# Kernel tuning notes

Hardware: AMD Instinct MI355X
Metric: run time of the kernel (lower is better)

## Reference

```python
import jax, jax.numpy as jnp
import numpy as np

H = 56; W = 56; WS = 7; SHIFT = 3; C = 256; NH = 8
HD = C // NH; N = WS * WS; NW = (H // WS) * (W // WS)
SCALE = HD ** -0.5
LN_EPS = 1e-5


def _rel_pos_index():
    coords = np.stack(np.meshgrid(np.arange(WS), np.arange(WS), indexing='ij'))  # (2, ws, ws)
    cf = coords.reshape(2, -1)
    rel = (cf[:, :, None] - cf[:, None, :]).transpose(1, 2, 0)  # (N, N, 2)
    rel[..., 0] += WS - 1
    rel[..., 1] += WS - 1
    rel[..., 0] *= 2 * WS - 1
    return rel.sum(-1)  # (N, N) indices into (2*ws-1)^2 table

RPI = jnp.asarray(_rel_pos_index())


def _attn_mask():
    img = np.zeros((H, W))
    slices = (slice(0, -WS), slice(-WS, -SHIFT), slice(-SHIFT, None))
    cnt = 0
    for hs in slices:
        for ws_ in slices:
            img[hs, ws_] = cnt
            cnt += 1
    mw = img.reshape(H // WS, WS, W // WS, WS).transpose(0, 2, 1, 3).reshape(-1, N)
    diff = mw[:, None, :] - mw[:, :, None]  # (nW, N, N), [w,i,j] = mw[w,j]-mw[w,i]
    return jnp.asarray(np.where(diff != 0, -100.0, 0.0).astype(np.float32))

AMASK = _attn_mask()  # (nW, N, N)


def ln(x, g, b):
    m = x.mean(-1, keepdims=True)
    v = x.var(-1, keepdims=True)
    return (x - m) / jnp.sqrt(v + LN_EPS) * g + b


def win_part(x):  # (B, H, W, C) -> (B*nW, N, C)
    B = x.shape[0]
    return x.reshape(B, H // WS, WS, W // WS, WS, C).transpose(0, 1, 3, 2, 4, 5).reshape(-1, N, C)


def win_rev(xw, B):  # (B*nW, N, C) -> (B, H, W, C)
    return xw.reshape(B, H // WS, W // WS, WS, WS, C).transpose(0, 1, 3, 2, 4, 5).reshape(B, H, W, C)


def setup_inputs() -> dict:
    key = jax.random.key(0)
    ks = iter(jax.random.split(key, 40))
    B, L = 16, H * W
    Ch = int(C * 4.0)
    p = {}
    p['x'] = jax.random.normal(next(ks), (B, L, C), jnp.float32)
    p['x_SAR'] = jax.random.normal(next(ks), (B, L, C), jnp.float32)
    p['ln1_g'] = jnp.ones((C,)); p['ln1_b'] = jnp.zeros((C,))
    p['ln1s_g'] = jnp.ones((C,)); p['ln1s_b'] = jnp.zeros((C,))
    p['qkv_w'] = jax.random.normal(next(ks), (3 * C, C)) * 0.02
    p['qkv_b'] = jnp.zeros((3 * C,))
    p['qkvs_w'] = jax.random.normal(next(ks), (3 * C, C)) * 0.02
    p['qkvs_b'] = jnp.zeros((3 * C,))
    p['rpb_table'] = jax.random.normal(next(ks), ((2 * WS - 1) ** 2, NH)) * 0.02
    p['fuse_w'] = jax.random.normal(next(ks), (NH, NH)) * 0.1  # Conv2d(8,8,1) weight squeezed
    p['fuse_b'] = jnp.zeros((NH,))
    p['proj_w'] = jax.random.normal(next(ks), (C, C)) * 0.02
    p['proj_b'] = jnp.zeros((C,))
    p['projs_w'] = jax.random.normal(next(ks), (C, C)) * 0.02
    p['projs_b'] = jnp.zeros((C,))
    p['ln2_g'] = jnp.ones((C,)); p['ln2_b'] = jnp.zeros((C,))
    p['ln2s_g'] = jnp.ones((C,)); p['ln2s_b'] = jnp.zeros((C,))
    p['fc1_w'] = jax.random.normal(next(ks), (Ch, C)) * 0.02
    p['fc1_b'] = jnp.zeros((Ch,))
    p['fc2_w'] = jax.random.normal(next(ks), (C, Ch)) * 0.02
    p['fc2_b'] = jnp.zeros((C,))
    p['fc1s_w'] = jax.random.normal(next(ks), (Ch, C)) * 0.02
    p['fc1s_b'] = jnp.zeros((Ch,))
    p['fc2s_w'] = jax.random.normal(next(ks), (C, Ch)) * 0.02
    p['fc2s_b'] = jnp.zeros((C,))
    return p


def reference(x, x_SAR, ln1_g, ln1_b, ln1s_g, ln1s_b, qkv_w, qkv_b, qkvs_w, qkvs_b,
              rpb_table, fuse_w, fuse_b, proj_w, proj_b, projs_w, projs_b,
              ln2_g, ln2_b, ln2s_g, ln2s_b, fc1_w, fc1_b, fc2_w, fc2_b,
              fc1s_w, fc1s_b, fc2s_w, fc2s_b):
    B = x.shape[0]
    sc, sc_s = x, x_SAR

    def pre(xx, g, b):  # norm -> spatial -> cyclic shift -> windows
        xs = ln(xx, g, b).reshape(B, H, W, C)
        xs = jnp.roll(xs, (-SHIFT, -SHIFT), axis=(1, 2))
        return win_part(xs)

    xw = pre(x, ln1_g, ln1_b)
    xws = pre(x_SAR, ln1s_g, ln1s_b)

    def qkv_f(xin, Wt, bt):
        qkv = (xin @ Wt.T + bt).reshape(-1, N, 3, NH, HD).transpose(2, 0, 3, 1, 4)
        return qkv[0], qkv[1], qkv[2]  # each (B*nW, nH, N, HD)

    q, k, v = qkv_f(xw, qkv_w, qkv_b)
    qs, ks_, vs = qkv_f(xws, qkvs_w, qkvs_b)

    attn = jnp.einsum('bhnd,bhmd->bhnm', q * SCALE, k)
    attn_s = jnp.einsum('bhnd,bhmd->bhnm', qs * SCALE, ks_)

    rpb = rpb_table[RPI.reshape(-1)].reshape(N, N, NH).transpose(2, 0, 1)  # (nH, N, N)
    attn = attn + rpb[None]
    attn_s = attn_s + rpb[None]

    # shift-window mask add
    attn = (attn.reshape(B, NW, NH, N, N) + AMASK[None, :, None]).reshape(-1, NH, N, N)
    attn_s = (attn_s.reshape(B, NW, NH, N, N) + AMASK[None, :, None]).reshape(-1, NH, N, N)

    # dual-branch fusion: 1x1 conv over head dim + sigmoid gate
    diff = attn_s - attn
    gate = jax.nn.sigmoid(jnp.einsum('oh,bhnm->bonm', fuse_w, diff) + fuse_b[None, :, None, None])
    attn_f = jax.nn.softmax(attn + diff * gate, axis=-1)
    attn_s = jax.nn.softmax(attn_s, axis=-1)

    def out_f(a, vv, pw, pb):
        o = jnp.einsum('bhnm,bhmd->bhnd', a, vv).transpose(0, 2, 1, 3).reshape(-1, N, C)
        return o @ pw.T + pb

    xo = out_f(attn_f, v, proj_w, proj_b)
    xos = out_f(attn_s, vs, projs_w, projs_b)

    def post(xout, scc, g2, b2, w1, b1, w2, b2m):
        xr = jnp.roll(win_rev(xout, B), (SHIFT, SHIFT), axis=(1, 2)).reshape(B, -1, C)
        xr = scc + xr
        h = jax.nn.gelu(ln(xr, g2, b2) @ w1.T + b1, approximate=False)
        return xr + (h @ w2.T + b2m)

    out = post(xo, sc, ln2_g, ln2_b, fc1_w, fc1_b, fc2_w, fc2_b)
    out_s = post(xos, sc_s, ln2s_g, ln2s_b, fc1s_w, fc1s_b, fc2s_w, fc2s_b)
    return out, out_s
```

## Files before the change

kernel.cpp:

```cpp
#include <hip/hip_runtime.h>
#include <hip/hip_bf16.h>
#include <cstdio>

typedef unsigned short ushort_t;
using bf16x8  = __attribute__((ext_vector_type(8))) __bf16;
using floatx4 = __attribute__((ext_vector_type(4))) float;

constexpr int    kTokens = 50176;
constexpr size_t TCsz    = (size_t)kTokens * 256;
constexpr float  kScale  = 0.17677669529663687f;
constexpr int    SPITCH  = 56;
constexpr size_t SPAIR   = 49 * 56;
constexpr size_t SBUFSZ  = (size_t)8192 * SPAIR;

__device__ __forceinline__ float bf2f(ushort_t u) {
  unsigned int x = (unsigned int)u << 16;
  return __uint_as_float(x);
}
__device__ __forceinline__ ushort_t f2bf(float f) {
  __hip_bfloat16 h = __float2bfloat16(f);
  return *(ushort_t*)&h;
}

__global__ __launch_bounds__(256) void f2b_k(const float* __restrict__ src,
                                             ushort_t* __restrict__ dst, int n) {
  int i = blockIdx.x * 256 + threadIdx.x;
  if (i < n) dst[i] = f2bf(src[i]);
}

__global__ __launch_bounds__(256) void bias_k(const float* __restrict__ rpb,
                                              float* __restrict__ bias,
                                              ushort_t* __restrict__ guard) {
  const int cls = blockIdx.x >> 3, head = blockIdx.x & 7;
  const int wh7 = cls >> 1, ww7 = cls & 1;
  float* bp = bias + (size_t)blockIdx.x * SPAIR;
  for (int e = threadIdx.x; e < (int)SPAIR; e += 256) {
    const int i = e / SPITCH, j = e % SPITCH;
    float val = 0.0f;
    if (j < 49) {
      const int yi = i / 7, xi = i % 7, yj = j / 7, xj = j % 7;
      val = rpb[((yi - yj + 6) * 13 + (xi - xj + 6)) * 8 + head];
      const int li = (wh7 ? (yi < 4 ? 1 : 2) : 0) * 3 + (ww7 ? (xi < 4 ? 1 : 2) : 0);
      const int lj = (wh7 ? (yj < 4 ? 1 : 2) : 0) * 3 + (ww7 ? (xj < 4 ? 1 : 2) : 0);
      if (li != lj) val -= 100.0f;
    }
    bp[e] = val;
  }
  if (blockIdx.x == 0 && threadIdx.x < 64) guard[threadIdx.x] = 0;
}

template <int SHIFTED>
__global__ __launch_bounds__(256) void ln_k(const float* __restrict__ x,
                                            const float* __restrict__ g,
                                            const float* __restrict__ b,
                                            ushort_t* __restrict__ yout) {
  const int wave = threadIdx.x >> 6, lane = threadIdx.x & 63;
  const int t = blockIdx.x * 4 + wave;
  size_t src;
  if (SHIFTED) {
    int bb = t / 3136, r = t % 3136;
    int wi = r / 49, n = r % 49;
    int hp = (wi >> 3) * 7 + n / 7;
    int wp = (wi & 7) * 7 + n % 7;
    int sh = hp + 3; if (sh >= 56) sh -= 56;
    int sw = wp + 3; if (sw >= 56) sw -= 56;
    src = ((size_t)bb * 3136 + sh * 56 + sw) * 256;
  } else {
    src = (size_t)t * 256;
  }
  const float4 v4 = *(const float4*)(x + src + lane * 4);
  float s  = v4.x + v4.y + v4.z + v4.w;
  float s2 = v4.x * v4.x + v4.y * v4.y + v4.z * v4.z + v4.w * v4.w;
#pragma unroll
  for (int off = 32; off > 0; off >>= 1) {
    s  += __shfl_xor(s,  off);
    s2 += __shfl_xor(s2, off);
  }
  const float mean = s * (1.0f / 256.0f);
  const float var  = s2 * (1.0f / 256.0f) - mean * mean;
  const float rstd = rsqrtf(var + 1e-5f);
  const float4 g4 = *(const float4*)(g + lane * 4);
  const float4 b4 = *(const float4*)(b + lane * 4);
  ushort4 o;
  o.x = f2bf((v4.x - mean) * rstd * g4.x + b4.x);
  o.y = f2bf((v4.y - mean) * rstd * g4.y + b4.y);
  o.z = f2bf((v4.z - mean) * rstd * g4.z + b4.z);
  o.w = f2bf((v4.w - mean) * rstd * g4.w + b4.w);
  *(ushort4*)(yout + (size_t)t * 256 + lane * 4) = o;
}

template <int MODE>
__global__ __launch_bounds__(256) void bgemm_k(const ushort_t* __restrict__ A,
                                               const ushort_t* __restrict__ W,
                                               const float* __restrict__ bias,
                                               float* __restrict__ outf,
                                               ushort_t* __restrict__ outb,
                                               const float* __restrict__ aux,
                                               int K, int Nc) {
  __shared__ __align__(16) ushort_t As[4][128][8];
  __shared__ __align__(16) ushort_t Bs[4][128][8];
  const int tid  = threadIdx.x;
  const int m0   = blockIdx.y * 128;
  const int n0   = blockIdx.x * 128;
  const int lane = tid & 63, wv = tid >> 6;
  const int wm   = (wv >> 1) * 64, wn = (wv & 1) * 64;
  const int l16  = lane & 15, quad = lane >> 4;
  const int srow = tid >> 2;
  const int skc  = tid & 3;

  floatx4 acc[4][4] = {};
  const ushort_t* Ap0 = A + (size_t)(m0 + srow) * K + skc * 8;
  const ushort_t* Ap1 = A + (size_t)(m0 + 64 + srow) * K + skc * 8;
  const ushort_t* Wp0 = W + (size_t)(n0 + srow) * K + skc * 8;
  const ushort_t* Wp1 = W + (size_t)(n0 + 64 + srow) * K + skc * 8;

  for (int k0 = 0; k0 < K; k0 += 32) {
    uint4 a0 = *(const uint4*)(Ap0 + k0);
    uint4 a1 = *(const uint4*)(Ap1 + k0);
    uint4 b0 = *(const uint4*)(Wp0 + k0);
    uint4 b1 = *(const uint4*)(Wp1 + k0);
    *(uint4*)&As[skc][srow][0]      = a0;
    *(uint4*)&As[skc][srow + 64][0] = a1;
    *(uint4*)&Bs[skc][srow][0]      = b0;
    *(uint4*)&Bs[skc][srow + 64][0] = b1;
    __syncthreads();
    bf16x8 af[4], bfr[4];
#pragma unroll
    for (int t = 0; t < 4; ++t) {
      af[t]  = *(const bf16x8*)&As[quad][wm + t * 16 + l16][0];
      bfr[t] = *(const bf16x8*)&Bs[quad][wn + t * 16 + l16][0];
    }
#pragma unroll
    for (int mt = 0; mt < 4; ++mt)
#pragma unroll
      for (int nt = 0; nt < 4; ++nt)
        acc[mt][nt] = __builtin_amdgcn_mfma_f32_16x16x32_bf16(af[mt], bfr[nt], acc[mt][nt], 0, 0, 0);
    __syncthreads();
  }

#pragma unroll
  for (int nt = 0; nt < 4; ++nt) {
    const int col = n0 + wn + nt * 16 + l16;
    const float bv = bias[col];
#pragma unroll
    for (int mt = 0; mt < 4; ++mt) {
#pragma unroll
      for (int r = 0; r < 4; ++r) {
        const int row = m0 + wm + mt * 16 + quad * 4 + r;
        float val = acc[mt][nt][r] + bv;
        if (MODE == 0) {
          const int which = col >> 8, head = (col >> 5) & 7, d = col & 31;
          if (which == 0) val *= kScale;
          const int wi = row / 49, n = row % 49;
          outb[(size_t)which * TCsz + (size_t)(wi * 8 + head) * 1568 + n * 32 + d] = f2bf(val);
        } else if (MODE == 1) {
          const int wi = row / 49, n = row % 49;
          const int b = wi >> 6, wl = wi & 63;
          const int hp = (wl >> 3) * 7 + n / 7;
          const int wp = (wl & 7) * 7 + n % 7;
          int h = hp + 3; if (h >= 56) h -= 56;
          int w = wp + 3; if (w >= 56) w -= 56;
          const size_t idx = ((size_t)(b * 3136 + h * 56 + w)) * 256 + col;
          outf[idx] = aux[idx] + val;
        } else if (MODE == 2) {
          val = 0.5f * val * (1.0f + erff(val * 0.70710678118654752f));
          outb[(size_t)row * Nc + col] = f2bf(val);
        } else {
          const size_t idx = (size_t)row * 256 + col;
          outf[idx] = aux[idx] + val;
        }
      }
    }
  }
}

__global__ __launch_bounds__(256) void scores_mfma_k(const ushort_t* __restrict__ q,
                                                     const ushort_t* __restrict__ k,
                                                     const float* __restrict__ bias,
                                                     ushort_t* __restrict__ S) {
  const int tid = threadIdx.x, lane = tid & 63, wv = tid >> 6;
  const int pair = blockIdx.x * 4 + wv;
  const int head = pair & 7, win = pair >> 3;
  const int l16 = lane & 15, quad = lane >> 4;
  const ushort_t* qb = q + (size_t)pair * 1568;
  const ushort_t* kb = k + (size_t)pair * 1568;
  bf16x8 af[4], bfr[4];
#pragma unroll
  for (int t = 0; t < 4; ++t) {
    af[t]  = *(const bf16x8*)(qb + (t * 16 + l16) * 32 + quad * 8);
    bfr[t] = *(const bf16x8*)(kb + (t * 16 + l16) * 32 + quad * 8);
  }
  floatx4 acc[4][4] = {};
#pragma unroll
  for (int mt = 0; mt < 4; ++mt)
#pragma unroll
    for (int nt = 0; nt < 4; ++nt)
      acc[mt][nt] = __builtin_amdgcn_mfma_f32_16x16x32_bf16(af[mt], bfr[nt], acc[mt][nt], 0, 0, 0);

  const int wl = win & 63;
  const int cls = (((wl >> 3) == 7) ? 2 : 0) + (((wl & 7) == 7) ? 1 : 0);
  const float* bp = bias + (size_t)(cls * 8 + head) * SPAIR;
  ushort_t* Sp = S + (size_t)pair * SPAIR;
#pragma unroll
  for (int nt = 0; nt < 4; ++nt) {
    const int col = nt * 16 + l16;
    if (col >= SPITCH) continue;
#pragma unroll
    for (int mt = 0; mt < 4; ++mt) {
#pragma unroll
      for (int r = 0; r < 4; ++r) {
        const int row = mt * 16 + quad * 4 + r;
        if (row >= 49) continue;
        const float val = (col < 49) ? acc[mt][nt][r] + bp[row * SPITCH + col] : 0.0f;
        Sp[row * SPITCH + col] = f2bf(val);
      }
    }
  }
}

__global__ __launch_bounds__(256) void fuse2_k(ushort_t* __restrict__ S,
                                               ushort_t* __restrict__ Ss,
                                               const float* __restrict__ fw,
                                               const float* __restrict__ fb) {
  __shared__ float s[8][637], ss[8][637];
  __shared__ float fwl[64], fbl[8];
  const int w = blockIdx.x >> 2, ch = blockIdx.x & 3;
  const int n0 = ch * 13;
  const int rows = (n0 + 13 <= 49) ? 13 : (49 - n0);
  const int cnt = 8 * rows * 49;
  const int tid = threadIdx.x;
  if (tid < 64) fwl[tid] = fw[tid];
  if (tid < 8)  fbl[tid] = fb[tid];
  for (int t = tid; t < cnt; t += 256) {
    const int h = t / (rows * 49), rm = t % (rows * 49);
    const int r = rm / 49, c = rm - r * 49;
    const size_t gaddr = (size_t)(w * 8 + h) * SPAIR + (size_t)(n0 + r) * SPITCH + c;
    s[h][rm]  = bf2f(S[gaddr]);
    ss[h][rm] = bf2f(Ss[gaddr]);
  }
  __syncthreads();
  for (int p = tid; p < rows * 49; p += 256) {
    float d[8];
#pragma unroll
    for (int h = 0; h < 8; ++h) d[h] = ss[h][p] - s[h][p];
#pragma unroll
    for (int o = 0; o < 8; ++o) {
      float g = fbl[o];
#pragma unroll
      for (int h = 0; h < 8; ++h) g = fmaf(fwl[o * 8 + h], d[h], g);
      g = 1.0f / (1.0f + expf(-g));
      s[o][p] = s[o][p] + d[o] * g;
    }
  }
  __syncthreads();
  if (tid < 16 * rows) {
    const int br = tid / (8 * rows);
    const int hr = tid % (8 * rows);
    const int h = hr / rows, r = hr % rows;
    float* row = (br ? ss[h] : s[h]) + r * 49;
    float mx = -1e30f;
    for (int m = 0; m < 49; ++m) mx = fmaxf(mx, row[m]);
    float sum = 0.0f;
    for (int m = 0; m < 49; ++m) { float e = expf(row[m] - mx); row[m] = e; sum += e; }
    const float inv = 1.0f / sum;
    for (int m = 0; m < 49; ++m) row[m] *= inv;
  }
  __syncthreads();
  for (int t = tid; t < cnt; t += 256) {
    const int h = t / (rows * 49), rm = t % (rows * 49);
    const int r = rm / 49, c = rm - r * 49;
    const size_t gaddr = (size_t)(w * 8 + h) * SPAIR + (size_t)(n0 + r) * SPITCH + c;
    S[gaddr]  = f2bf(s[h][rm]);
    Ss[gaddr] = f2bf(ss[h][rm]);
  }
}

__global__ __launch_bounds__(256) void pv_mfma_k(const ushort_t* __restrict__ P,
                                                 const ushort_t* __restrict__ v,
                                                 ushort_t* __restrict__ O) {
  __shared__ __align__(16) ushort_t vt[4][32][72];
  const int tid = threadIdx.x, lane = tid & 63, wv = tid >> 6;
  const int pair = blockIdx.x * 4 + wv;
  const int head = pair & 7, win = pair >> 3;
  const int l16 = lane & 15, quad = lane >> 4;
  const ushort_t* vb = v + (size_t)pair * 1568;
  for (int e = lane; e < 736; e += 64) {
    const int d = e / 23, m = 49 + e % 23;
    vt[wv][d][m] = 0;
  }
  for (int e = lane; e < 1568; e += 64) {
    vt[wv][e & 31][e >> 5] = vb[e];
  }
  __syncthreads();
  bf16x8 bfr[2][2];
#pragma unroll
  for (int nt = 0; nt < 2; ++nt)
#pragma unroll
    for (int ks = 0; ks < 2; ++ks)
      bfr[nt][ks] = *(const bf16x8*)&vt[wv][nt * 16 + l16][ks * 32 + quad * 8];

  const ushort_t* Pb = P + (size_t)pair * SPAIR;
  floatx4 acc[4][2] = {};
#pragma unroll
  for (int ks = 0; ks < 2; ++ks) {
#pragma unroll
    for (int mt = 0; mt < 4; ++mt) {
      const bf16x8 af = *(const bf16x8*)(Pb + (size_t)(mt * 16 + l16) * SPITCH + ks * 32 + quad * 8);
#pragma unroll
      for (int nt = 0; nt < 2; ++nt)
        acc[mt][nt] = __builtin_amdgcn_mfma_f32_16x16x32_bf16(af, bfr[nt][ks], acc[mt][nt], 0, 0, 0);
    }
  }
#pragma unroll
  for (int mt = 0; mt < 4; ++mt) {
#pragma unroll
    for (int r = 0; r < 4; ++r) {
      const int n = mt * 16 + quad * 4 + r;
      if (n >= 49) continue;
      const size_t base = ((size_t)(win * 49 + n)) * 256 + head * 32;
#pragma unroll
      for (int nt = 0; nt < 2; ++nt)
        O[base + nt * 16 + l16] = f2bf(acc[mt][nt][r]);
    }
  }
}

extern "C" void kernel_launch(void* const* d_in, const int* in_sizes, int n_in,
                              void* d_out, int out_size, void* d_ws, size_t ws_size,
                              hipStream_t stream) {
  if (n_in < 29) { fprintf(stderr, "kernel_launch: expected 29 inputs, got %d\n", n_in); return; }
  const float* x      = (const float*)d_in[0];
  const float* xsar   = (const float*)d_in[1];
  const float* ln1_g  = (const float*)d_in[2];
  const float* ln1_b  = (const float*)d_in[3];
  const float* ln1s_g = (const float*)d_in[4];
  const float* ln1s_b = (const float*)d_in[5];
  const float* qkv_w  = (const float*)d_in[6];
  const float* qkv_b  = (const float*)d_in[7];
  const float* qkvs_w = (const float*)d_in[8];
  const float* qkvs_b = (const float*)d_in[9];
  const float* rpb    = (const float*)d_in[10];
  const float* fuse_w = (const float*)d_in[11];
  const float* fuse_b = (const float*)d_in[12];
  const float* proj_w = (const float*)d_in[13];
  const float* proj_b = (const float*)d_in[14];
  const float* projs_w = (const float*)d_in[15];
  const float* projs_b = (const float*)d_in[16];
  const float* ln2_g  = (const float*)d_in[17];
  const float* ln2_b  = (const float*)d_in[18];
  const float* ln2s_g = (const float*)d_in[19];
  const float* ln2s_b = (const float*)d_in[20];
  const float* fc1_w  = (const float*)d_in[21];
  const float* fc1_b  = (const float*)d_in[22];
  const float* fc2_w  = (const float*)d_in[23];
  const float* fc2_b  = (const float*)d_in[24];
  const float* fc1s_w = (const float*)d_in[25];
  const float* fc1s_b = (const float*)d_in[26];
  const float* fc2s_w = (const float*)d_in[27];
  const float* fc2s_b = (const float*)d_in[28];
  float* out = (float*)d_out;
  float* ws  = (float*)d_ws;

  const size_t need = 8 * TCsz * sizeof(float);
  if (ws_size < need) {
    fprintf(stderr, "kernel_launch: ws_size %zu < needed %zu\n", ws_size, need);
    return;
  }

  ushort_t* H   = (ushort_t*)ws;
  ushort_t* xw  = H;
  ushort_t* xws = H + TCsz;
  ushort_t* q   = H + 2 * TCsz;
  ushort_t* qs  = H + 5 * TCsz;
  ushort_t* v_  = H + 4 * TCsz;
  ushort_t* vs  = H + 7 * TCsz;
  ushort_t* SA  = H + 8 * TCsz;
  ushort_t* SB  = SA + SBUFSZ;
  ushort_t* guard = SB + SBUFSZ;
  float* xr  = ws + 6 * TCsz;
  float* xrs = ws + 7 * TCsz;
  ushort_t* y   = H + 2 * TCsz;
  ushort_t* ysb = H + 3 * TCsz;
  ushort_t* hbuf = H + 4 * TCsz;
  ushort_t* wb  = H + 12 * TCsz - 1572864;
  float* biasbuf = (float*)(H + 12 * TCsz - 1572864 - 175616);
  ushort_t* wqkv  = wb;
  ushort_t* wqkvs = wb + 196608;
  ushort_t* wproj = wb + 393216;
  ushort_t* wprojs= wb + 458752;
  ushort_t* wfc1  = wb + 524288;
  ushort_t* wfc1s = wb + 786432;
  ushort_t* wfc2  = wb + 1048576;
  ushort_t* wfc2s = wb + 1310720;

  f2b_k<<<768, 256, 0, stream>>>(qkv_w,  wqkv,  196608);
  f2b_k<<<768, 256, 0, stream>>>(qkvs_w, wqkvs, 196608);
  f2b_k<<<256, 256, 0, stream>>>(proj_w, wproj, 65536);
  f2b_k<<<256, 256, 0, stream>>>(projs_w,wprojs,65536);
  f2b_k<<<1024,256, 0, stream>>>(fc1_w,  wfc1,  262144);
  f2b_k<<<1024,256, 0, stream>>>(fc1s_w, wfc1s, 262144);
  f2b_k<<<1024,256, 0, stream>>>(fc2_w,  wfc2,  262144);
  f2b_k<<<1024,256, 0, stream>>>(fc2s_w, wfc2s, 262144);
  bias_k<<<32, 256, 0, stream>>>(rpb, biasbuf, guard);

  ln_k<1><<<12544, 256, 0, stream>>>(x,    ln1_g,  ln1_b,  xw);
  ln_k<1><<<12544, 256, 0, stream>>>(xsar, ln1s_g, ln1s_b, xws);
  bgemm_k<0><<<dim3(6, 392), 256, 0, stream>>>(xw,  wqkv,  qkv_b,  nullptr, q,  nullptr, 256, 768);
  bgemm_k<0><<<dim3(6, 392), 256, 0, stream>>>(xws, wqkvs, qkvs_b, nullptr, qs, nullptr, 256, 768);
  scores_mfma_k<<<2048, 256, 0, stream>>>(q,  q + TCsz,  biasbuf, SA);
  scores_mfma_k<<<2048, 256, 0, stream>>>(qs, qs + TCsz, biasbuf, SB);
  fuse2_k<<<4096, 256, 0, stream>>>(SA, SB, fuse_w, fuse_b);
  pv_mfma_k<<<2048, 256, 0, stream>>>(SA, v_, H);
  pv_mfma_k<<<2048, 256, 0, stream>>>(SB, vs, H + TCsz);
  bgemm_k<1><<<dim3(2, 392), 256, 0, stream>>>(H,          wproj,  proj_b,  xr,  nullptr, x,    256, 256);
  bgemm_k<1><<<dim3(2, 392), 256, 0, stream>>>(H + TCsz,   wprojs, projs_b, xrs, nullptr, xsar, 256, 256);
  ln_k<0><<<12544, 256, 0, stream>>>(xr,  ln2_g,  ln2_b,  y);
  ln_k<0><<<12544, 256, 0, stream>>>(xrs, ln2s_g, ln2s_b, ysb);
  bgemm_k<2><<<dim3(8, 392), 256, 0, stream>>>(y,    wfc1,  fc1_b,  nullptr, hbuf, nullptr, 256, 1024);
  bgemm_k<3><<<dim3(2, 392), 256, 0, stream>>>(hbuf, wfc2,  fc2_b,  out,     nullptr, xr,  1024, 256);
  bgemm_k<2><<<dim3(8, 392), 256, 0, stream>>>(ysb,  wfc1s, fc1s_b, nullptr, hbuf, nullptr, 256, 1024);
  bgemm_k<3><<<dim3(2, 392), 256, 0, stream>>>(hbuf, wfc2s, fc2s_b, out + TCsz, nullptr, xrs, 1024, 256);
}
```

Baseline: 1.022 ms.

## Load GEMM tiles directly to LDS with swizzle, XCD-aware block remap, hoist epilogue indexing

The GEMM kernel now uses global_load_lds to move A and W tiles straight into shared memory without passing through registers. It stores them in an XOR-swizzled row-major layout to avoid bank conflicts, and reads fragments through the matching swizzle. Workgroups are remapped so that neighbouring tiles land on the same XCD for better L2 reuse. The epilogues precompute per-row output offsets once instead of redoing div/mod for every element. The risks are correctness of the swizzle and lane mapping in the direct-to-LDS path, and the loop still has no double buffering.

New measurement: 969.9 us. -5.1%, faster.

```diff
diff --git a/kernel.cpp b/kernel.cpp
--- a/kernel.cpp
+++ b/kernel.cpp
@@ -20,6 +20,12 @@
 __device__ __forceinline__ ushort_t f2bf(float f) {
   __hip_bfloat16 h = __float2bfloat16(f);
   return *(ushort_t*)&h;
+}
+
+__device__ __forceinline__ void gl_lds16(const ushort_t* g, ushort_t* l) {
+  __builtin_amdgcn_global_load_lds(
+      (const __attribute__((address_space(1))) unsigned int*)g,
+      (__attribute__((address_space(3))) unsigned int*)l, 16, 0, 0);
 }
 
 __global__ __launch_bounds__(256) void f2b_k(const float* __restrict__ src,
@@ -97,38 +103,51 @@
                                                ushort_t* __restrict__ outb,
                                                const float* __restrict__ aux,
                                                int K, int Nc) {
-  __shared__ __align__(16) ushort_t As[4][128][8];
-  __shared__ __align__(16) ushort_t Bs[4][128][8];
-  const int tid  = threadIdx.x;
-  const int m0   = blockIdx.y * 128;
-  const int n0   = blockIdx.x * 128;
+  __shared__ __align__(16) ushort_t As[128 * 32];
+  __shared__ __align__(16) ushort_t Bs[128 * 32];
+  const int tid = threadIdx.x;
+  const int nbx = gridDim.x;
+  const int nwg = nbx * gridDim.y;
+  int flat = blockIdx.y * nbx + blockIdx.x;
+  {
+    const int xcd = flat & 7, idx = flat >> 3;
+    const int q8 = nwg >> 3, r8 = nwg & 7;
+    flat = (xcd < r8 ? xcd * (q8 + 1) : r8 * (q8 + 1) + (xcd - r8) * q8) + idx;
+  }
+  const int m0 = (flat / nbx) * 128;
+  const int n0 = (flat % nbx) * 128;
   const int lane = tid & 63, wv = tid >> 6;
-  const int wm   = (wv >> 1) * 64, wn = (wv & 1) * 64;
-  const int l16  = lane & 15, quad = lane >> 4;
+  const int wm = (wv >> 1) * 64, wn = (wv & 1) * 64;
+  const int l16 = lane & 15, quad = lane >> 4;
+
   const int srow = tid >> 2;
-  const int skc  = tid & 3;
+  const int gkc  = (tid & 3) ^ ((tid >> 3) & 3);
+  const ushort_t* Ag0 = A + (size_t)(m0 + srow) * K + gkc * 8;
+  const ushort_t* Ag1 = A + (size_t)(m0 + 64 + srow) * K + gkc * 8;
+  const ushort_t* Wg0 = W + (size_t)(n0 + srow) * K + gkc * 8;
+  const ushort_t* Wg1 = W + (size_t)(n0 + 64 + srow) * K + gkc * 8;
+  ushort_t* AsW0 = As + wv * 512;
+  ushort_t* AsW1 = As + 2048 + wv * 512;
+  ushort_t* BsW0 = Bs + wv * 512;
+  ushort_t* BsW1 = Bs + 2048 + wv * 512;
+
+  const int kcq = quad ^ ((l16 >> 1) & 3);
+  const int arA = (wm + l16) * 32 + kcq * 8;
+  const int arB = (wn + l16) * 32 + kcq * 8;
 
   floatx4 acc[4][4] = {};
-  const ushort_t* Ap0 = A + (size_t)(m0 + srow) * K + skc * 8;
-  const ushort_t* Ap1 = A + (size_t)(m0 + 64 + srow) * K + skc * 8;
-  const ushort_t* Wp0 = W + (size_t)(n0 + srow) * K + skc * 8;
-  const ushort_t* Wp1 = W + (size_t)(n0 + 64 + srow) * K + skc * 8;
-
   for (int k0 = 0; k0 < K; k0 += 32) {
-    uint4 a0 = *(const uint4*)(Ap0 + k0);
-    uint4 a1 = *(const uint4*)(Ap1 + k0);
-    uint4 b0 = *(const uint4*)(Wp0 + k0);
-    uint4 b1 = *(const uint4*)(Wp1 + k0);
-    *(uint4*)&As[skc][srow][0]      = a0;
-    *(uint4*)&As[skc][srow + 64][0] = a1;
-    *(uint4*)&Bs[skc][srow][0]      = b0;
-    *(uint4*)&Bs[skc][srow + 64][0] = b1;
+    gl_lds16(Ag0, AsW0);
+    gl_lds16(Ag1, AsW1);
+    gl_lds16(Wg0, BsW0);
+    gl_lds16(Wg1, BsW1);
+    Ag0 += 32; Ag1 += 32; Wg0 += 32; Wg1 += 32;
     __syncthreads();
     bf16x8 af[4], bfr[4];
 #pragma unroll
     for (int t = 0; t < 4; ++t) {
-      af[t]  = *(const bf16x8*)&As[quad][wm + t * 16 + l16][0];
-      bfr[t] = *(const bf16x8*)&Bs[quad][wn + t * 16 + l16][0];
+      af[t]  = *(const bf16x8*)&As[arA + t * 512];
+      bfr[t] = *(const bf16x8*)&Bs[arB + t * 512];
     }
 #pragma unroll
     for (int mt = 0; mt < 4; ++mt)
@@ -138,37 +157,86 @@
     __syncthreads();
   }
 
-#pragma unroll
-  for (int nt = 0; nt < 4; ++nt) {
-    const int col = n0 + wn + nt * 16 + l16;
-    const float bv = bias[col];
+  if (MODE == 0) {
+    size_t rb[16];
+#pragma unroll
+    for (int mt = 0; mt < 4; ++mt) {
+      int row = m0 + wm + mt * 16 + quad * 4;
+      int wi = row / 49, n = row - wi * 49;
+#pragma unroll
+      for (int r = 0; r < 4; ++r) {
+        rb[mt * 4 + r] = (size_t)wi * 12544 + (size_t)n * 32;
+        if (++n == 49) { n = 0; ++wi; }
+      }
+    }
+#pragma unroll
+    for (int nt = 0; nt < 4; ++nt) {
+      const int col = n0 + wn + nt * 16 + l16;
+      const int which = col >> 8, head = (col >> 5) & 7, d = col & 31;
+      const float bv = bias[col];
+      const float sc = (which == 0) ? kScale : 1.0f;
+      ushort_t* ob = outb + (size_t)which * TCsz + head * 1568 + d;
+#pragma unroll
+      for (int i = 0; i < 16; ++i)
+        ob[rb[i]] = f2bf((acc[i >> 2][nt][i & 3] + bv) * sc);
+    }
+  } else if (MODE == 1) {
+    size_t rb[16];
 #pragma unroll
     for (int mt = 0; mt < 4; ++mt) {
 #pragma unroll
       for (int r = 0; r < 4; ++r) {
         const int row = m0 + wm + mt * 16 + quad * 4 + r;
-        float val = acc[mt][nt][r] + bv;
-        if (MODE == 0) {
-          const int which = col >> 8, head = (col >> 5) & 7, d = col & 31;
-          if (which == 0) val *= kScale;
-          const int wi = row / 49, n = row % 49;
-          outb[(size_t)which * TCsz + (size_t)(wi * 8 + head) * 1568 + n * 32 + d] = f2bf(val);
-        } else if (MODE == 1) {
-          const int wi = row / 49, n = row % 49;
-          const int b = wi >> 6, wl = wi & 63;
-          const int hp = (wl >> 3) * 7 + n / 7;
-          const int wp = (wl & 7) * 7 + n % 7;
-          int h = hp + 3; if (h >= 56) h -= 56;
-          int w = wp + 3; if (w >= 56) w -= 56;
-          const size_t idx = ((size_t)(b * 3136 + h * 56 + w)) * 256 + col;
-          outf[idx] = aux[idx] + val;
-        } else if (MODE == 2) {
-          val = 0.5f * val * (1.0f + erff(val * 0.70710678118654752f));
-          outb[(size_t)row * Nc + col] = f2bf(val);
-        } else {
-          const size_t idx = (size_t)row * 256 + col;
-          outf[idx] = aux[idx] + val;
-        }
+        const int wi = row / 49, n = row - wi * 49;
+        const int b = wi >> 6, wl = wi & 63;
+        int h = (wl >> 3) * 7 + n / 7 + 3; if (h >= 56) h -= 56;
+        int w = (wl & 7) * 7 + n % 7 + 3; if (w >= 56) w -= 56;
+        rb[mt * 4 + r] = ((size_t)(b * 3136 + h * 56 + w)) * 256;
+      }
+    }
+#pragma unroll
+    for (int nt = 0; nt < 4; ++nt) {
+      const int col = n0 + wn + nt * 16 + l16;
+      const float bv = bias[col];
+#pragma unroll
+      for (int i = 0; i < 16; ++i) {
+        const size_t idx = rb[i] + col;
+        outf[idx] = aux[idx] + acc[i >> 2][nt][i & 3] + bv;
+      }
+    }
+  } else if (MODE == 2) {
+    size_t rb[16];
+#pragma unroll
+    for (int mt = 0; mt < 4; ++mt)
+#pragma unroll
+      for (int r = 0; r < 4; ++r)
+        rb[mt * 4 + r] = (size_t)(m0 + wm + mt * 16 + quad * 4 + r) * Nc;
+#pragma unroll
+    for (int nt = 0; nt < 4; ++nt) {
+      const int col = n0 + wn + nt * 16 + l16;
+      const float bv = bias[col];
+#pragma unroll
+      for (int i = 0; i < 16; ++i) {
+        float val = acc[i >> 2][nt][i & 3] + bv;
+        val = 0.5f * val * (1.0f + erff(val * 0.70710678118654752f));
+        outb[rb[i] + col] = f2bf(val);
+      }
+    }
+  } else {
+    size_t rb[16];
+#pragma unroll
+    for (int mt = 0; mt < 4; ++mt)
+#pragma unroll
+      for (int r = 0; r < 4; ++r)
+        rb[mt * 4 + r] = (size_t)(m0 + wm + mt * 16 + quad * 4 + r) * 256;
+#pragma unroll
+    for (int nt = 0; nt < 4; ++nt) {
+      const int col = n0 + wn + nt * 16 + l16;
+      const float bv = bias[col];
+#pragma unroll
+      for (int i = 0; i < 16; ++i) {
+        const size_t idx = rb[i] + col;
+        outf[idx] = aux[idx] + acc[i >> 2][nt][i & 3] + bv;
       }
     }
   }
```
